# Kernel tuning notes

Measured on AMD Instinct MI355X. Metric: run time of the kernel, lower is better.

The kernel has to match this reference:

```python
import jax, jax.numpy as jnp
import numpy as np
from jax import lax

B, S, V, E, H, T = 64, 256, 50000, 300, 256, 13  # H = hidden per direction (512//2)


def setup_inputs() -> dict:
    key = jax.random.key(0)
    ks = iter(jax.random.split(key, 48))
    def rn(shape, s=0.05):
        return jax.random.normal(next(ks), shape, jnp.float32) * s
    inp = {}
    inp["x"] = jax.random.randint(next(ks), (B, S), 0, V)
    inp["pos"] = jax.random.normal(next(ks), (B, S), jnp.float32)
    inp["emb"] = rn((V, E), 1.0)
    # LSTM layer 0 (input E=300), layer 1 (input 2H=512); [dir, 4H, in]/[dir,4H,H]/[dir,4H]
    inp["lstm_Wih0"] = rn((2, 4 * H, E))
    inp["lstm_Whh0"] = rn((2, 4 * H, H))
    inp["lstm_b0"] = rn((2, 4 * H))
    inp["lstm_Wih1"] = rn((2, 4 * H, 2 * H))
    inp["lstm_Whh1"] = rn((2, 4 * H, H))
    inp["lstm_b1"] = rn((2, 4 * H))
    # PositionFeedForward (dim_model = hidden = S = 256)
    inp["pos_fc1_w"] = rn((S, S)); inp["pos_fc1_b"] = rn((S,))
    inp["pos_fc2_w"] = rn((S, S)); inp["pos_fc2_b"] = rn((S,))
    inp["pos_ln_g"] = jnp.ones((S,)); inp["pos_ln_b"] = jnp.zeros((S,))
    # conditionLinear: hidden_size(512) -> pad_size(256), stored [in,out]
    inp["cond_w"] = rn((2 * H, S)); inp["cond_b"] = rn((S,))
    # ConditionalLayerNorm(pad_size)
    inp["cln_weight"] = jnp.ones((S,)); inp["cln_bias"] = jnp.zeros((S,))
    inp["cln_wd"] = rn((S, S)); inp["cln_bd"] = rn((S, S))
    # SelfAttention(pad_size) on the [B,S] sentence vector
    inp["att_wq"] = rn((S, S)); inp["att_bq"] = rn((S,))
    inp["att_wk"] = rn((S, S)); inp["att_bk"] = rn((S,))
    inp["att_wv"] = rn((S, S)); inp["att_bv"] = rn((S,))
    inp["att_ln_g"] = jnp.ones((S,)); inp["att_ln_b"] = jnp.zeros((S,))
    # attLinear: pad_size -> 1
    inp["attlin_w"] = rn((S, 1)); inp["attlin_b"] = rn((1,))
    # final linear: pad_size -> tag_num
    inp["out_w"] = rn((S, T)); inp["out_b"] = rn((T,))
    # CRF params
    inp["crf_start"] = rn((T,), 0.1)
    inp["crf_end"] = rn((T,), 0.1)
    inp["crf_trans"] = rn((T, T), 0.1)
    return inp


def _layer_norm(x, g, b, eps=1e-5):
    m = jnp.mean(x, -1, keepdims=True)
    v = jnp.mean((x - m) ** 2, -1, keepdims=True)
    return (x - m) / jnp.sqrt(v + eps) * g + b


def _lstm_dir(x, Wih, Whh, b, reverse):
    # x: [B,S,in] -> hs [B,S,H]; PyTorch gate order i,f,g,o
    xt = jnp.swapaxes(x, 0, 1)  # [S,B,in]
    xg = jnp.einsum('sbi,gi->sbg', xt, Wih) + b  # precompute input gates [S,B,4H]
    def step(carry, g_in):
        h, c = carry
        g = g_in + h @ Whh.T
        i, f, gg, o = jnp.split(g, 4, axis=-1)
        c = jax.nn.sigmoid(f) * c + jax.nn.sigmoid(i) * jnp.tanh(gg)
        h = jax.nn.sigmoid(o) * jnp.tanh(c)
        return (h, c), h
    init = (jnp.zeros((x.shape[0], H), x.dtype), jnp.zeros((x.shape[0], H), x.dtype))
    _, hs = lax.scan(step, init, xg, reverse=reverse)
    return jnp.swapaxes(hs, 0, 1)


def _bilstm_layer(x, Wih, Whh, b):
    fwd = _lstm_dir(x, Wih[0], Whh[0], b[0], False)
    bwd = _lstm_dir(x, Wih[1], Whh[1], b[1], True)
    return jnp.concatenate([fwd, bwd], axis=-1)


def _viterbi(em, start, end, trans):
    # em: [B,S,T] -> best tag path [B,S] (full-length mask, as in torchcrf decode)
    score0 = start + em[:, 0]  # [B,T]
    def step(score, em_t):
        nxt = score[:, :, None] + trans[None] + em_t[:, None, :]  # [B,T,T]
        return jnp.max(nxt, axis=1), jnp.argmax(nxt, axis=1)
    score, hist = lax.scan(step, score0, jnp.swapaxes(em[:, 1:], 0, 1))  # hist [S-1,B,T]
    last = jnp.argmax(score + end, axis=-1)  # [B]
    def back(tag, idx_t):
        prev = jnp.take_along_axis(idx_t, tag[:, None], axis=1)[:, 0]
        return prev, prev
    _, tags_rev = lax.scan(back, last, hist, reverse=True)  # [S-1,B]
    tags = jnp.concatenate([tags_rev, last[None]], axis=0)  # [S,B]
    return jnp.swapaxes(tags, 0, 1)


def reference(x, pos, emb, lstm_Wih0, lstm_Whh0, lstm_b0, lstm_Wih1, lstm_Whh1, lstm_b1,
              pos_fc1_w, pos_fc1_b, pos_fc2_w, pos_fc2_b, pos_ln_g, pos_ln_b,
              cond_w, cond_b, cln_weight, cln_bias, cln_wd, cln_bd,
              att_wq, att_bq, att_wk, att_bk, att_wv, att_bv, att_ln_g, att_ln_b,
              attlin_w, attlin_b, out_w, out_b, crf_start, crf_end, crf_trans):
    out = emb[x]  # [B,S,E]
    out = _bilstm_layer(out, lstm_Wih0, lstm_Whh0, lstm_b0)  # [B,S,2H]
    out = _bilstm_layer(out, lstm_Wih1, lstm_Whh1, lstm_b1)  # [B,S,2H]
    # PositionFeedForward on pos [B,S]
    h = jax.nn.relu(pos @ pos_fc1_w + pos_fc1_b) @ pos_fc2_w + pos_fc2_b
    pos_out = _layer_norm(h + pos, pos_ln_g, pos_ln_b)
    # conditionLinear: [B,S,2H] -> [B,S,S]
    out = out @ cond_w + cond_b
    # ConditionalLayerNorm with cond=pos_out, eps=1e-12
    cond = pos_out[:, None, :]  # [B,1,S]
    w = cond @ cln_wd.T + cln_weight  # weight_dense is Linear(no bias): c @ W.T; stored square, use .T
    bb = cond @ cln_bd.T + cln_bias
    mean = jnp.mean(out, -1, keepdims=True)
    cen = out - mean
    var = jnp.mean(cen ** 2, -1, keepdims=True)
    out = cen / jnp.sqrt(var + 1e-12) * w + bb
    # sentence attention over [B,S]
    sentence = (out @ attlin_w + attlin_b)[..., 0]  # [B,S]
    Q = sentence @ att_wq + att_bq
    K = sentence @ att_wk + att_bk
    Vv = sentence @ att_wv + att_bv
    alpha = jax.nn.softmax(Q * K / jnp.sqrt(jnp.float32(S)), axis=-1)
    att = _layer_norm(alpha * Vv, att_ln_g, att_ln_b)  # [B,S]
    out = out * att[:, :, None]
    logits = out @ out_w + out_b  # [B,S,T]
    tag = _viterbi(logits, crf_start, crf_end, crf_trans)
    return (logits, tag)
```

## Files before the change

kernel.cpp:

```cpp
#include <hip/hip_runtime.h>
#include <math.h>

#define B_    64
#define S_    256
#define E_    300
#define H_    256
#define T_    13
#define G4_   1024
#define D2H_  512

typedef short bf16x8 __attribute__((ext_vector_type(8)));
typedef float f32x4  __attribute__((ext_vector_type(4)));
typedef unsigned short u16;
typedef unsigned long long u64;

__device__ __forceinline__ float sigf(float x)   { return __builtin_amdgcn_rcpf(1.f + __expf(-x)); }
__device__ __forceinline__ float tanhf_(float x) { return __builtin_amdgcn_rcpf(1.f + __expf(-2.f*x))*2.f - 1.f; }

__device__ __forceinline__ u16 f2bf(float f) {
  union { float f; unsigned u; } v; v.f = f;
  unsigned r = v.u + 0x7fff + ((v.u >> 16) & 1);
  return (u16)(r >> 16);
}
__device__ __forceinline__ float bf2f(u16 h) {
  union { unsigned u; float f; } v; v.u = ((unsigned)h) << 16;
  return v.f;
}

__device__ __forceinline__ u64 cload64(const u64* p) {
  return __hip_atomic_load(p, __ATOMIC_RELAXED, __HIP_MEMORY_SCOPE_AGENT);
}
__device__ __forceinline__ void cstore32(unsigned* p, unsigned v) {
  __hip_atomic_store(p, v, __ATOMIC_RELAXED, __HIP_MEMORY_SCOPE_AGENT);
}

__global__ __launch_bounds__(64)
void k_embed(const int* __restrict__ x, const float* __restrict__ emb,
             u16* __restrict__ oh, u16* __restrict__ ol) {
  int bs = blockIdx.x;
  int xv = x[bs];
  const float4* src = (const float4*)(emb + (size_t)xv * E_);
  u64* dh = (u64*)(oh + (size_t)bs * 320);
  u64* dl = (u64*)(ol + (size_t)bs * 320);
  for (int q = threadIdx.x; q < 80; q += 64) {
    float4 v = (q < 75) ? src[q] : make_float4(0.f, 0.f, 0.f, 0.f);
    u16 hh[4], ll[4];
    float vv[4] = {v.x, v.y, v.z, v.w};
    #pragma unroll
    for (int j = 0; j < 4; j++) {
      hh[j] = f2bf(vv[j]);
      ll[j] = f2bf(vv[j] - bf2f(hh[j]));
    }
    dh[q] = (u64)hh[0] | ((u64)hh[1] << 16) | ((u64)hh[2] << 32) | ((u64)hh[3] << 48);
    dl[q] = (u64)ll[0] | ((u64)ll[1] << 16) | ((u64)ll[2] << 32) | ((u64)ll[3] << 48);
  }
}

__global__ __launch_bounds__(256)
void k_cvtbf2(const float* __restrict__ w, u16* __restrict__ hi, u16* __restrict__ lo, int n) {
  int i = blockIdx.x * 256 + threadIdx.x;
  if (i < n) {
    float v = w[i];
    u16 h = f2bf(v);
    hi[i] = h;
    lo[i] = f2bf(v - bf2f(h));
  }
}

__global__ __launch_bounds__(256)
void k_cvtpad(const float* __restrict__ w, u16* __restrict__ hi, u16* __restrict__ lo,
              int Ksrc, int Kpad) {
  int r = blockIdx.x;
  for (int k = threadIdx.x; k < Kpad; k += 256) {
    float v = (k < Ksrc) ? w[(size_t)r * Ksrc + k] : 0.f;
    u16 h = f2bf(v);
    hi[(size_t)r * Kpad + k] = h;
    lo[(size_t)r * Kpad + k] = f2bf(v - bf2f(h));
  }
}

__global__ __launch_bounds__(256)
void k_cvtT(const float* __restrict__ w, u16* __restrict__ hi, u16* __restrict__ lo) {
  int n = blockIdx.x;
  for (int k = threadIdx.x; k < 512; k += 256) {
    float v = w[(size_t)k * 256 + n];
    u16 h = f2bf(v);
    hi[(size_t)n * 512 + k] = h;
    lo[(size_t)n * 512 + k] = f2bf(v - bf2f(h));
  }
}

__global__ __launch_bounds__(256)
void k_bgemm(const u16* __restrict__ Ahi, const u16* __restrict__ Alo,
             const u16* __restrict__ Whi, const u16* __restrict__ Wlo,
             const float* __restrict__ bias, float* __restrict__ C,
             int K, int N, int permute, long wStride, long bStride, long cStride)
{
  __shared__ u16 Ash[2][128 * 40];
  __shared__ u16 Wsh[2][128 * 40];

  int tid = threadIdx.x;
  int d   = blockIdx.z;
  int n0  = blockIdx.x * 128, m0 = blockIdx.y * 128;
  int lane = tid & 63;
  int w    = tid >> 6;
  int l15  = lane & 15;
  int quad = lane >> 4;
  int mh = (w >> 1) * 64, nh = (w & 1) * 64;

  int comp = tid >> 7, row = tid & 127;
  int gr = m0 + row;
  int ar = permute ? ((gr & 63) * S_ + (gr >> 6)) : gr;
  const u16* Asrc = (comp ? Alo : Ahi) + (size_t)ar * K;
  const u16* Wsrc = (comp ? Wlo : Whi) + (size_t)d * wStride + (size_t)(n0 + row) * K;
  u16* AshC = &Ash[comp][row * 40];
  u16* WshC = &Wsh[comp][row * 40];

  f32x4 acc[4][4];
  #pragma unroll
  for (int mt = 0; mt < 4; mt++)
    #pragma unroll
    for (int nt = 0; nt < 4; nt++) acc[mt][nt] = (f32x4)(0.f);

  for (int k0 = 0; k0 < K; k0 += 32) {
    float4 a0 = *(const float4*)(Asrc + k0);
    float4 a1 = *(const float4*)(Asrc + k0 + 8);
    float4 a2 = *(const float4*)(Asrc + k0 + 16);
    float4 a3 = *(const float4*)(Asrc + k0 + 24);
    float4 w0 = *(const float4*)(Wsrc + k0);
    float4 w1 = *(const float4*)(Wsrc + k0 + 8);
    float4 w2 = *(const float4*)(Wsrc + k0 + 16);
    float4 w3 = *(const float4*)(Wsrc + k0 + 24);
    __syncthreads();
    *(float4*)(AshC)      = a0; *(float4*)(AshC + 8)  = a1;
    *(float4*)(AshC + 16) = a2; *(float4*)(AshC + 24) = a3;
    *(float4*)(WshC)      = w0; *(float4*)(WshC + 8)  = w1;
    *(float4*)(WshC + 16) = w2; *(float4*)(WshC + 24) = w3;
    __syncthreads();

    bf16x8 ah[4], al[4], bh[4], bl[4];
    #pragma unroll
    for (int mt = 0; mt < 4; mt++) {
      int rr = mh + mt * 16 + l15;
      ah[mt] = *(const bf16x8*)&Ash[0][rr * 40 + quad * 8];
      al[mt] = *(const bf16x8*)&Ash[1][rr * 40 + quad * 8];
    }
    #pragma unroll
    for (int nt = 0; nt < 4; nt++) {
      int rr = nh + nt * 16 + l15;
      bh[nt] = *(const bf16x8*)&Wsh[0][rr * 40 + quad * 8];
      bl[nt] = *(const bf16x8*)&Wsh[1][rr * 40 + quad * 8];
    }
    #pragma unroll
    for (int mt = 0; mt < 4; mt++)
      #pragma unroll
      for (int nt = 0; nt < 4; nt++) {
        acc[mt][nt] = __builtin_amdgcn_mfma_f32_16x16x32_bf16(ah[mt], bh[nt], acc[mt][nt], 0, 0, 0);
        acc[mt][nt] = __builtin_amdgcn_mfma_f32_16x16x32_bf16(ah[mt], bl[nt], acc[mt][nt], 0, 0, 0);
        acc[mt][nt] = __builtin_amdgcn_mfma_f32_16x16x32_bf16(al[mt], bh[nt], acc[mt][nt], 0, 0, 0);
      }
  }

  const float* biasd = bias + (size_t)d * bStride;
  float* Cd = C + (size_t)d * cStride;
  #pragma unroll
  for (int nt = 0; nt < 4; nt++) {
    int cn = n0 + nh + nt * 16 + l15;
    float bv = biasd[cn];
    #pragma unroll
    for (int mt = 0; mt < 4; mt++) {
      int mr = m0 + mh + mt * 16 + quad * 4;
      #pragma unroll
      for (int j = 0; j < 4; j++)
        Cd[(size_t)(mr + j) * N + cn] = acc[mt][nt][j] + bv;
    }
  }
}

__global__ __launch_bounds__(256, 1)
void k_lstm_mfma(const float* __restrict__ xg,
                 const u16* __restrict__ Whi, const u16* __restrict__ Wlo,
                 u16* __restrict__ houth, u16* __restrict__ houtl,
                 u16* __restrict__ hb_hi, u16* __restrict__ hb_lo,
                 unsigned* __restrict__ flags, unsigned magic)
{
  __shared__ __align__(16) u16   hsh[4 * 256];
  __shared__ __align__(16) u16   hsl[4 * 256];
  __shared__ __align__(16) float gl[4 * 16 * 34];

  int tid  = threadIdx.x;
  int us   = blockIdx.x & 7;
  int bg   = (blockIdx.x >> 3) & 15;
  int d    = blockIdx.x >> 7;
  int lane = tid & 63;
  int gate = tid >> 6;
  int l15  = lane & 15;
  int quad = lane >> 4;
  int bpc  = l15 & 3;

  bf16x8 afh[2][8], afl[2][8];
  {
    const u16* WbH = Whi + ((size_t)d * G4_ + gate * 256 + us * 32 + l15) * H_;
    const u16* WbL = Wlo + ((size_t)d * G4_ + gate * 256 + us * 32 + l15) * H_;
    #pragma unroll
    for (int mt = 0; mt < 2; mt++)
      #pragma unroll
      for (int kt = 0; kt < 8; kt++) {
        afh[mt][kt] = *(const bf16x8*)(WbH + (size_t)mt * 16 * H_ + kt * 32 + quad * 8);
        afl[mt][kt] = *(const bf16x8*)(WbL + (size_t)mt * 16 * H_ + kt * 32 + quad * 8);
      }
  }

  float c0 = 0.f, c1 = 0.f;
  int sb = tid >> 6;
  int cw = tid & 63;
  int sch = cw >> 1, shalf = cw & 1;
  int scc = sch ^ sb;
  int bc = tid & 3, uo2 = (tid >> 2) * 2;

  const float* xgd = xg + (size_t)d * S_ * B_ * G4_;
  size_t isl = (size_t)(d * 16 + bg) * S_ * 4 * 256;
  u16* hbh = hb_hi + isl;
  u16* hbl = hb_lo + isl;
  unsigned* fl = flags + (d * 16 + bg) * S_ * 8;

  for (int it = 0; it < S_; it++) {
    int s = d ? (S_ - 1 - it) : it;

    f32x4 acc[2];
    const float* xgrow = xgd + (size_t)s * B_ * G4_ + (size_t)(bg * 4 + bpc) * G4_
                       + gate * 256 + us * 32;
    acc[0] = *(const f32x4*)(xgrow + quad * 4);
    acc[1] = *(const f32x4*)(xgrow + 16 + quad * 4);

    if (it > 0) {
      if (tid < 8) {
        const unsigned* f = &fl[(it - 1) * 8 + tid];
        while (__hip_atomic_load(f, __ATOMIC_RELAXED, __HIP_MEMORY_SCOPE_AGENT) != magic)
          __builtin_amdgcn_s_sleep(1);
      }
      __syncthreads();

      {
        u64 th = cload64((const u64*)(hbh + (size_t)(it - 1) * 1024) + tid);
        u64 tl = cload64((const u64*)(hbl + (size_t)(it - 1) * 1024) + tid);
        *(u64*)&hsh[sb * 256 + scc * 8 + shalf * 4] = th;
        *(u64*)&hsl[sb * 256 + scc * 8 + shalf * 4] = tl;
      }
      __syncthreads();

      #pragma unroll
      for (int kt = 0; kt < 8; kt++) {
        int cc = (kt * 4 + quad) ^ bpc;
        bf16x8 bh = *(const bf16x8*)&hsh[bpc * 256 + cc * 8];
        bf16x8 bl = *(const bf16x8*)&hsl[bpc * 256 + cc * 8];
        #pragma unroll
        for (int mt = 0; mt < 2; mt++) {
          acc[mt] = __builtin_amdgcn_mfma_f32_16x16x32_bf16(afh[mt][kt], bh, acc[mt], 0, 0, 0);
          acc[mt] = __builtin_amdgcn_mfma_f32_16x16x32_bf16(afh[mt][kt], bl, acc[mt], 0, 0, 0);
          acc[mt] = __builtin_amdgcn_mfma_f32_16x16x32_bf16(afl[mt][kt], bh, acc[mt], 0, 0, 0);
        }
      }
    }

    #pragma unroll
    for (int mt = 0; mt < 2; mt++)
      *(f32x4*)&gl[(gate * 16 + l15) * 34 + mt * 16 + quad * 4] = acc[mt];
    __syncthreads();

    if (tid < 64) {
      float2 vi = *(const float2*)&gl[(0 * 16 + bc) * 34 + uo2];
      float2 vf = *(const float2*)&gl[(1 * 16 + bc) * 34 + uo2];
      float2 vg = *(const float2*)&gl[(2 * 16 + bc) * 34 + uo2];
      float2 vo = *(const float2*)&gl[(3 * 16 + bc) * 34 + uo2];
      c0 = sigf(vf.x) * c0 + sigf(vi.x) * tanhf_(vg.x);
      c1 = sigf(vf.y) * c1 + sigf(vi.y) * tanhf_(vg.y);
      float h0 = sigf(vo.x) * tanhf_(c0);
      float h1 = sigf(vo.y) * tanhf_(c1);

      u16 h0h = f2bf(h0), h1h = f2bf(h1);
      u16 h0l = f2bf(h0 - bf2f(h0h)), h1l = f2bf(h1 - bf2f(h1h));
      unsigned phv = (unsigned)h0h | ((unsigned)h1h << 16);
      unsigned plv = (unsigned)h0l | ((unsigned)h1l << 16);

      size_t ho = ((size_t)(bg * 4 + bc) * S_ + s) * D2H_ + d * H_ + us * 32 + uo2;
      *(unsigned*)(houth + ho) = phv;
      *(unsigned*)(houtl + ho) = plv;

      size_t hoff = (size_t)it * 1024 + bc * 256 + us * 32 + uo2;
      cstore32((unsigned*)(hbh + hoff), phv);
      cstore32((unsigned*)(hbl + hoff), plv);
    }

    __syncthreads();
    if (tid == 0)
      __hip_atomic_store(&fl[it * 8 + us], magic, __ATOMIC_RELAXED, __HIP_MEMORY_SCOPE_AGENT);
  }
}

__device__ __forceinline__ float bsum(float v, float* sb) {
  int t = threadIdx.x;
  sb[t] = v; __syncthreads();
  for (int s = 128; s; s >>= 1) { if (t < s) sb[t] += sb[t + s]; __syncthreads(); }
  float r = sb[0]; __syncthreads(); return r;
}
__device__ __forceinline__ float bmax(float v, float* sb) {
  int t = threadIdx.x;
  sb[t] = v; __syncthreads();
  for (int s = 128; s; s >>= 1) { if (t < s) sb[t] = fmaxf(sb[t], sb[t + s]); __syncthreads(); }
  float r = sb[0]; __syncthreads(); return r;
}

__global__ __launch_bounds__(256)
void k_pos(const float* __restrict__ pos, const float* __restrict__ fc1w, const float* __restrict__ fc1b,
           const float* __restrict__ fc2w, const float* __restrict__ fc2b,
           const float* __restrict__ lng, const float* __restrict__ lnb, float* __restrict__ pos_out)
{
  __shared__ float sp[256], sh[256], sb[256];
  int b = blockIdx.x, t = threadIdx.x;
  sp[t] = pos[b * 256 + t];
  __syncthreads();
  float a1 = fc1b[t];
  for (int s = 0; s < 256; s++) a1 += sp[s] * fc1w[s * 256 + t];
  a1 = fmaxf(a1, 0.f);
  sh[t] = a1; __syncthreads();
  float a2 = fc2b[t] + sp[t];
  for (int s = 0; s < 256; s++) a2 += sh[s] * fc2w[s * 256 + t];
  float m   = bsum(a2, sb) * (1.f / 256.f);
  float cen = a2 - m;
  float var = bsum(cen * cen, sb) * (1.f / 256.f);
  pos_out[b * 256 + t] = cen * rsqrtf(var + 1e-5f) * lng[t] + lnb[t];
}

__global__ __launch_bounds__(256)
void k_clnA(const float* __restrict__ pos_out, const float* __restrict__ wd, const float* __restrict__ bd,
            const float* __restrict__ cw, const float* __restrict__ cb,
            float* __restrict__ wvec, float* __restrict__ bbvec)
{
  __shared__ float sp[256];
  int b = blockIdx.x, t = threadIdx.x;
  sp[t] = pos_out[b * 256 + t];
  __syncthreads();
  const float4* wdr = (const float4*)(wd + (size_t)t * 256);
  const float4* bdr = (const float4*)(bd + (size_t)t * 256);
  float aw = 0.f, ab = 0.f;
  for (int q = 0; q < 64; q++) {
    float4 w4 = wdr[q], b4 = bdr[q];
    float s0 = sp[q*4], s1 = sp[q*4+1], s2 = sp[q*4+2], s3 = sp[q*4+3];
    aw += s0*w4.x + s1*w4.y + s2*w4.z + s3*w4.w;
    ab += s0*b4.x + s1*b4.y + s2*b4.z + s3*b4.w;
  }
  wvec [b * 256 + t] = aw + cw[t];
  bbvec[b * 256 + t] = ab + cb[t];
}

__global__ __launch_bounds__(256)
void k_clnB(const float* __restrict__ oc, const float* __restrict__ wvec, const float* __restrict__ bbvec,
            const float* __restrict__ alw, const float* __restrict__ alb,
            float* __restrict__ outn, float* __restrict__ sentence)
{
  __shared__ float sb[256];
  int bs = blockIdx.x, t = threadIdx.x;
  int b = bs >> 8;
  float v   = oc[(size_t)bs * 256 + t];
  float m   = bsum(v, sb) * (1.f / 256.f);
  float cen = v - m;
  float var = bsum(cen * cen, sb) * (1.f / 256.f);
  float o   = cen * rsqrtf(var + 1e-12f) * wvec[b * 256 + t] + bbvec[b * 256 + t];
  outn[(size_t)bs * 256 + t] = o;
  float sv = bsum(o * alw[t], sb);
  if (t == 0) sentence[bs] = sv + alb[0];
}

__global__ __launch_bounds__(256)
void k_att(const float* __restrict__ sentence,
           const float* __restrict__ wq, const float* __restrict__ bq,
           const float* __restrict__ wk, const float* __restrict__ bk,
           const float* __restrict__ wv, const float* __restrict__ bv,
           const float* __restrict__ lng, const float* __restrict__ lnb,
           float* __restrict__ att)
{
  __shared__ float ss[256], sb[256];
  int b = blockIdx.x, t = threadIdx.x;
  ss[t] = sentence[b * 256 + t];
  __syncthreads();
  float q = bq[t], k = bk[t], vv = bv[t];
  for (int s = 0; s < 256; s++) {
    float sv = ss[s];
    q  += sv * wq[s * 256 + t];
    k  += sv * wk[s * 256 + t];
    vv += sv * wv[s * 256 + t];
  }
  float x  = q * k * (1.f / 16.f);
  float mx = bmax(x, sb);
  float e  = expf(x - mx);
  float sm = bsum(e, sb);
  float a  = (e / sm) * vv;
  float m   = bsum(a, sb) * (1.f / 256.f);
  float cen = a - m;
  float var = bsum(cen * cen, sb) * (1.f / 256.f);
  att[b * 256 + t] = cen * rsqrtf(var + 1e-5f) * lng[t] + lnb[t];
}

__global__ __launch_bounds__(64)
void k_out(const float* __restrict__ outn, const float* __restrict__ att,
           const float* __restrict__ ow, const float* __restrict__ ob,
           float* __restrict__ logits)
{
  __shared__ float row[256];
  int bs = blockIdx.x, t = threadIdx.x;
  ((float4*)row)[t] = ((const float4*)(outn + (size_t)bs * 256))[t];
  __syncthreads();
  float a = att[bs];
  if (t < T_) {
    float acc = 0.f;
    for (int c = 0; c < 256; c++) acc += row[c] * ow[c * T_ + t];
    logits[(size_t)bs * T_ + t] = a * acc + ob[t];
  }
}

__global__ __launch_bounds__(64)
void k_viterbi(const float* __restrict__ logits, const float* __restrict__ start,
               const float* __restrict__ endv, const float* __restrict__ trans,
               float* __restrict__ tags)
{
  __shared__ float sc[16];
  __shared__ float str[169];
  __shared__ unsigned char hist[255 * 13];
  __shared__ int tg[256];
  int b = blockIdx.x, t = threadIdx.x;
  for (int i = t; i < 169; i += 64) str[i] = trans[i];
  if (t < 13) sc[t] = start[t] + logits[((size_t)b * 256) * 13 + t];
  __syncthreads();
  for (int s = 1; s < 256; s++) {
    float best = -1e30f; int bi = 0;
    if (t < 13) {
      best = sc[0] + str[t]; bi = 0;
      for (int i = 1; i < 13; i++) {
        float v = sc[i] + str[i * 13 + t];
        if (v > best) { best = v; bi = i; }
      }
    }
    __syncthreads();
    if (t < 13) {
      sc[t] = best + logits[((size_t)b * 256 + s) * 13 + t];
      hist[(s - 1) * 13 + t] = (unsigned char)bi;
    }
    __syncthreads();
  }
  if (t == 0) {
    float best = sc[0] + endv[0]; int last = 0;
    for (int j = 1; j < 13; j++) {
      float v = sc[j] + endv[j];
      if (v > best) { best = v; last = j; }
    }
    tg[255] = last;
    int cur = last;
    for (int s = 254; s >= 0; s--) { cur = hist[s * 13 + cur]; tg[s] = cur; }
  }
  __syncthreads();
  for (int s = t; s < 256; s += 64) tags[b * 256 + s] = (float)tg[s];
}

extern "C" void kernel_launch(void* const* d_in, const int* in_sizes, int n_in,
                              void* d_out, int out_size, void* d_ws, size_t ws_size,
                              hipStream_t stream)
{
  const int*   x     = (const int*)  d_in[0];
  const float* pos   = (const float*)d_in[1];
  const float* emb   = (const float*)d_in[2];
  const float* Wih0  = (const float*)d_in[3];
  const float* Whh0  = (const float*)d_in[4];
  const float* b0    = (const float*)d_in[5];
  const float* Wih1  = (const float*)d_in[6];
  const float* Whh1  = (const float*)d_in[7];
  const float* b1    = (const float*)d_in[8];
  const float* fc1w  = (const float*)d_in[9];
  const float* fc1b  = (const float*)d_in[10];
  const float* fc2w  = (const float*)d_in[11];
  const float* fc2b  = (const float*)d_in[12];
  const float* plng  = (const float*)d_in[13];
  const float* plnb  = (const float*)d_in[14];
  const float* condw = (const float*)d_in[15];
  const float* condb = (const float*)d_in[16];
  const float* clnw  = (const float*)d_in[17];
  const float* clnb  = (const float*)d_in[18];
  const float* clnwd = (const float*)d_in[19];
  const float* clnbd = (const float*)d_in[20];
  const float* wq    = (const float*)d_in[21];
  const float* bq    = (const float*)d_in[22];
  const float* wk    = (const float*)d_in[23];
  const float* bk    = (const float*)d_in[24];
  const float* wv    = (const float*)d_in[25];
  const float* bv    = (const float*)d_in[26];
  const float* atlng = (const float*)d_in[27];
  const float* atlnb = (const float*)d_in[28];
  const float* alw   = (const float*)d_in[29];
  const float* alb   = (const float*)d_in[30];
  const float* ow    = (const float*)d_in[31];
  const float* ob    = (const float*)d_in[32];
  const float* cstart= (const float*)d_in[33];
  const float* cend  = (const float*)d_in[34];
  const float* ctrans= (const float*)d_in[35];

  const size_t BS = (size_t)B_ * S_;
  float* ws = (float*)d_ws;
  float* r1   = ws;
  float* xg   = r1 + 5242880;
  float* l0r  = xg + 33554432;
  float* l1r  = l0r + 8388608;
  float* pos_out  = l1r + 8388608;
  float* wvec     = pos_out + 16384;
  float* bbvec    = wvec + 16384;
  float* sentence = bbvec + 16384;
  float* attv     = sentence + 16384;
  unsigned* flags = (unsigned*)(attv + 16384);
  u16* whhh0 = (u16*)(flags + 65536);
  u16* whhl0 = whhh0 + 524288;
  u16* whhh1 = whhl0 + 524288;
  u16* whhl1 = whhh1 + 524288;
  u16* wih0h = whhl1 + 524288;
  u16* wih0l = wih0h + 655360;
  u16* wih1h = wih0l + 655360;
  u16* wih1l = wih1h + 1048576;
  u16* condTh = wih1l + 1048576;
  u16* condTl = condTh + 131072;

  u16* embh = (u16*)r1;
  u16* embl = embh + 5242880;
  float* out_cond = r1;
  u16* l0h = (u16*)l0r;
  u16* l0l = l0h + 8388608;
  u16* l1h = (u16*)l1r;
  u16* l1l = l1h + 8388608;
  const size_t HBN = (size_t)32 * S_ * 4 * 256;
  u16* hb0 = (u16*)l1r;
  u16* hb1 = (u16*)l0r;
  float* outn = l0r;
  float* logits = (float*)d_out;
  float* tags   = logits + BS * T_;

  k_embed <<<dim3(B_ * S_), dim3(64), 0, stream>>>(x, emb, embh, embl);
  k_cvtbf2<<<dim3(2048), dim3(256), 0, stream>>>(Whh0, whhh0, whhl0, 2 * G4_ * H_);
  k_cvtbf2<<<dim3(2048), dim3(256), 0, stream>>>(Whh1, whhh1, whhl1, 2 * G4_ * H_);
  k_cvtpad<<<dim3(2048), dim3(256), 0, stream>>>(Wih0, wih0h, wih0l, 300, 320);
  k_cvtpad<<<dim3(2048), dim3(256), 0, stream>>>(Wih1, wih1h, wih1l, 512, 512);
  k_cvtT  <<<dim3(256),  dim3(256), 0, stream>>>(condw, condTh, condTl);

  k_bgemm<<<dim3(8, 128, 2), dim3(256), 0, stream>>>(
      embh, embl, wih0h, wih0l, b0, xg, 320, G4_, 1,
      (long)G4_ * 320, (long)G4_, (long)BS * G4_);
  k_lstm_mfma<<<dim3(256), dim3(256), 0, stream>>>(
      xg, whhh0, whhl0, l0h, l0l, hb0, hb0 + HBN, flags, 0x51A75A01u);

  k_bgemm<<<dim3(8, 128, 2), dim3(256), 0, stream>>>(
      l0h, l0l, wih1h, wih1l, b1, xg, 512, G4_, 1,
      (long)G4_ * 512, (long)G4_, (long)BS * G4_);
  k_lstm_mfma<<<dim3(256), dim3(256), 0, stream>>>(
      xg, whhh1, whhl1, l1h, l1l, hb1, hb1 + HBN, flags, 0x51A75A02u);

  k_bgemm<<<dim3(2, 128, 1), dim3(256), 0, stream>>>(
      l1h, l1l, condTh, condTl, condb, out_cond, 512, 256, 0, 0, 0, 0);

  k_pos <<<dim3(B_), dim3(256), 0, stream>>>(pos, fc1w, fc1b, fc2w, fc2b, plng, plnb, pos_out);
  k_clnA<<<dim3(B_), dim3(256), 0, stream>>>(pos_out, clnwd, clnbd, clnw, clnb, wvec, bbvec);
  k_clnB<<<dim3(B_ * S_), dim3(256), 0, stream>>>(out_cond, wvec, bbvec, alw, alb, outn, sentence);
  k_att <<<dim3(B_), dim3(256), 0, stream>>>(sentence, wq, bq, wk, bk, wv, bv, atlng, atlnb, attv);
  k_out <<<dim3(B_ * S_), dim3(64), 0, stream>>>(outn, attv, ow, ob, logits);
  k_viterbi<<<dim3(B_), dim3(64), 0, stream>>>(logits, cstart, cend, ctrans, tags);
}
```

Measured before the change: 1.677 ms.

## Replace flag-based LSTM step sync with sentinel-tagged data polling

The persistent LSTM kernel no longer publishes per-block flags after a barrier. Each h value pair is now written as one 64-bit hi/lo word into a buffer pre-filled with a sentinel, and consumers spin directly on the data until the sentinel is gone. The block's own slice is written straight into LDS instead of being round-tripped through global memory. This removes one barrier and the flag store/poll latency from every timestep. The cost is two extra memsets of the exchange buffers, and correctness now depends on real data never matching the 0x7F7F7F7F sentinel in the low 32 bits.

```diff
diff --git a/kernel.cpp b/kernel.cpp
--- a/kernel.cpp
+++ b/kernel.cpp
@@ -12,7 +12,10 @@
 typedef short bf16x8 __attribute__((ext_vector_type(8)));
 typedef float f32x4  __attribute__((ext_vector_type(4)));
 typedef unsigned short u16;
+typedef unsigned int   u32;
 typedef unsigned long long u64;
+
+#define SENT32 0x7F7F7F7Fu
 
 __device__ __forceinline__ float sigf(float x)   { return __builtin_amdgcn_rcpf(1.f + __expf(-x)); }
 __device__ __forceinline__ float tanhf_(float x) { return __builtin_amdgcn_rcpf(1.f + __expf(-2.f*x))*2.f - 1.f; }
@@ -30,7 +33,7 @@
 __device__ __forceinline__ u64 cload64(const u64* p) {
   return __hip_atomic_load(p, __ATOMIC_RELAXED, __HIP_MEMORY_SCOPE_AGENT);
 }
-__device__ __forceinline__ void cstore32(unsigned* p, unsigned v) {
+__device__ __forceinline__ void cstore64(u64* p, u64 v) {
   __hip_atomic_store(p, v, __ATOMIC_RELAXED, __HIP_MEMORY_SCOPE_AGENT);
 }
 
@@ -181,8 +184,7 @@
 void k_lstm_mfma(const float* __restrict__ xg,
                  const u16* __restrict__ Whi, const u16* __restrict__ Wlo,
                  u16* __restrict__ houth, u16* __restrict__ houtl,
-                 u16* __restrict__ hb_hi, u16* __restrict__ hb_lo,
-                 unsigned* __restrict__ flags, unsigned magic)
+                 u64* __restrict__ hbx)
 {
   __shared__ __align__(16) u16   hsh[4 * 256];
   __shared__ __align__(16) u16   hsl[4 * 256];
@@ -212,17 +214,18 @@
   }
 
   float c0 = 0.f, c1 = 0.f;
-  int sb = tid >> 6;
-  int cw = tid & 63;
-  int sch = cw >> 1, shalf = cw & 1;
-  int scc = sch ^ sb;
-  int bc = tid & 3, uo2 = (tid >> 2) * 2;
+
+  int pw_us = tid >> 5;
+  int pw_bc = (tid >> 3) & 3;
+  int pw_u  = pw_us * 32 + (tid & 7) * 4;
+  bool remote = (pw_us != us);
+  int pw_off = ((pw_bc * 256 + pw_u) * 2) ^ ((pw_bc & 1) << 6);
+
+  int bc = tid & 3, p = tid >> 2, uo2 = p * 2;
+  int self_off = ((bc * 256 + us * 32 + uo2) * 2) ^ ((bc & 1) << 6);
 
   const float* xgd = xg + (size_t)d * S_ * B_ * G4_;
-  size_t isl = (size_t)(d * 16 + bg) * S_ * 4 * 256;
-  u16* hbh = hb_hi + isl;
-  u16* hbl = hb_lo + isl;
-  unsigned* fl = flags + (d * 16 + bg) * S_ * 8;
+  u64* hb = hbx + (size_t)(d * 16 + bg) * S_ * 512;
 
   for (int it = 0; it < S_; it++) {
     int s = d ? (S_ - 1 - it) : it;
@@ -234,26 +237,25 @@
     acc[1] = *(const f32x4*)(xgrow + 16 + quad * 4);
 
     if (it > 0) {
-      if (tid < 8) {
-        const unsigned* f = &fl[(it - 1) * 8 + tid];
-        while (__hip_atomic_load(f, __ATOMIC_RELAXED, __HIP_MEMORY_SCOPE_AGENT) != magic)
+      if (remote) {
+        const u64* src = hb + (size_t)(it - 1) * 512 + tid * 2;
+        u64 a = cload64(src), b = cload64(src + 1);
+        while (((u32)a == SENT32) | ((u32)b == SENT32)) {
           __builtin_amdgcn_s_sleep(1);
+          a = cload64(src); b = cload64(src + 1);
+        }
+        u64 hi64 = (a & 0xFFFFFFFFull) | (b << 32);
+        u64 lo64 = (a >> 32) | (b & 0xFFFFFFFF00000000ull);
+        *(u64*)((char*)hsh + pw_off) = hi64;
+        *(u64*)((char*)hsl + pw_off) = lo64;
       }
       __syncthreads();
 
-      {
-        u64 th = cload64((const u64*)(hbh + (size_t)(it - 1) * 1024) + tid);
-        u64 tl = cload64((const u64*)(hbl + (size_t)(it - 1) * 1024) + tid);
-        *(u64*)&hsh[sb * 256 + scc * 8 + shalf * 4] = th;
-        *(u64*)&hsl[sb * 256 + scc * 8 + shalf * 4] = tl;
-      }
-      __syncthreads();
-
       #pragma unroll
       for (int kt = 0; kt < 8; kt++) {
-        int cc = (kt * 4 + quad) ^ bpc;
-        bf16x8 bh = *(const bf16x8*)&hsh[bpc * 256 + cc * 8];
-        bf16x8 bl = *(const bf16x8*)&hsl[bpc * 256 + cc * 8];
+        int coff = ((bpc * 256 + (kt * 4 + quad) * 8) * 2) ^ ((bpc & 1) << 6);
+        bf16x8 bh = *(const bf16x8*)((const char*)hsh + coff);
+        bf16x8 bl = *(const bf16x8*)((const char*)hsl + coff);
         #pragma unroll
         for (int mt = 0; mt < 2; mt++) {
           acc[mt] = __builtin_amdgcn_mfma_f32_16x16x32_bf16(afh[mt][kt], bh, acc[mt], 0, 0, 0);
@@ -280,21 +282,19 @@
 
       u16 h0h = f2bf(h0), h1h = f2bf(h1);
       u16 h0l = f2bf(h0 - bf2f(h0h)), h1l = f2bf(h1 - bf2f(h1h));
-      unsigned phv = (unsigned)h0h | ((unsigned)h1h << 16);
-      unsigned plv = (unsigned)h0l | ((unsigned)h1l << 16);
+      u32 phv = (u32)h0h | ((u32)h1h << 16);
+      u32 plv = (u32)h0l | ((u32)h1l << 16);
 
       size_t ho = ((size_t)(bg * 4 + bc) * S_ + s) * D2H_ + d * H_ + us * 32 + uo2;
-      *(unsigned*)(houth + ho) = phv;
-      *(unsigned*)(houtl + ho) = plv;
-
-      size_t hoff = (size_t)it * 1024 + bc * 256 + us * 32 + uo2;
-      cstore32((unsigned*)(hbh + hoff), phv);
-      cstore32((unsigned*)(hbl + hoff), plv);
-    }
-
-    __syncthreads();
-    if (tid == 0)
-      __hip_atomic_store(&fl[it * 8 + us], magic, __ATOMIC_RELAXED, __HIP_MEMORY_SCOPE_AGENT);
+      *(u32*)(houth + ho) = phv;
+      *(u32*)(houtl + ho) = plv;
+
+      *(u32*)((char*)hsh + self_off) = phv;
+      *(u32*)((char*)hsl + self_off) = plv;
+
+      cstore64(hb + (size_t)it * 512 + us * 64 + bc * 16 + p,
+               (u64)phv | ((u64)plv << 32));
+    }
   }
 }
 
@@ -533,12 +533,14 @@
   u16* l0l = l0h + 8388608;
   u16* l1h = (u16*)l1r;
   u16* l1l = l1h + 8388608;
-  const size_t HBN = (size_t)32 * S_ * 4 * 256;
-  u16* hb0 = (u16*)l1r;
-  u16* hb1 = (u16*)l0r;
+  u64* hb0 = (u64*)l1r;
+  u64* hb1 = (u64*)l0r;
+  const size_t HBBYTES = (size_t)32 * S_ * 512 * sizeof(u64);
   float* outn = l0r;
   float* logits = (float*)d_out;
   float* tags   = logits + BS * T_;
+
+  hipMemsetAsync(hb0, 0x7F, HBBYTES, stream);
 
   k_embed <<<dim3(B_ * S_), dim3(64), 0, stream>>>(x, emb, embh, embl);
   k_cvtbf2<<<dim3(2048), dim3(256), 0, stream>>>(Whh0, whhh0, whhl0, 2 * G4_ * H_);
@@ -551,13 +553,14 @@
       embh, embl, wih0h, wih0l, b0, xg, 320, G4_, 1,
       (long)G4_ * 320, (long)G4_, (long)BS * G4_);
   k_lstm_mfma<<<dim3(256), dim3(256), 0, stream>>>(
-      xg, whhh0, whhl0, l0h, l0l, hb0, hb0 + HBN, flags, 0x51A75A01u);
+      xg, whhh0, whhl0, l0h, l0l, hb0);
 
   k_bgemm<<<dim3(8, 128, 2), dim3(256), 0, stream>>>(
       l0h, l0l, wih1h, wih1l, b1, xg, 512, G4_, 1,
       (long)G4_ * 512, (long)G4_, (long)BS * G4_);
+  hipMemsetAsync(hb1, 0x7F, HBBYTES, stream);
   k_lstm_mfma<<<dim3(256), dim3(256), 0, stream>>>(
-      xg, whhh1, whhl1, l1h, l1l, hb1, hb1 + HBN, flags, 0x51A75A02u);
+      xg, whhh1, whhl1, l1h, l1l, hb1);
 
   k_bgemm<<<dim3(2, 128, 1), dim3(256), 0, stream>>>(
       l1h, l1l, condTh, condTl, condb, out_cond, 512, 256, 0, 0, 0, 0);
```

Measured after the change: 1.609 ms. 4.1% less time.
